# Performance work log

Measured on AMD Instinct MI355X. Metric: run time of the kernel, lower is better.

The kernel has to match this reference:

```python
import jax, jax.numpy as jnp
import numpy as np

VOL = (256, 256, 256)
K = 64  # number of connected components (clusters)


def setup_inputs() -> dict:
    key = jax.random.key(0)
    k1, k2, k3 = jax.random.split(key, 3)
    # Precomputed connected-component labels of (pred + target) > 0.
    # 0 = background, 1..K = clusters.
    labels = jax.random.randint(k1, VOL, 0, K + 1, dtype=jnp.int32)
    fg = labels > 0
    # Binary prediction / ground-truth masks, nonzero only inside labeled regions
    # (consistent with labels being components of the overlay of pred and target).
    pred = ((jax.random.uniform(k2, VOL) < 0.6) & fg).astype(jnp.float32)
    target = ((jax.random.uniform(k3, VOL) < 0.6) & fg).astype(jnp.float32)
    return {"pred": pred, "target": target, "labels": labels, "num_clusters": K}


def reference(pred, target, labels, num_clusters):
    # Per-cluster dice via one fused segment reduction instead of a Python loop
    # over clusters. Segment 0 is background and is dropped, matching
    # range(1, num_features + 1) in the original.
    lab = labels.reshape(-1)
    p = pred.reshape(-1)
    t = target.reshape(-1)
    nseg = num_clusters + 1
    # intersection = sum(pred_cluster * gt_cluster); pred/target are binary so
    # logical_and(...).float() products reduce to pred * target per segment.
    inter = jax.ops.segment_sum(p * t, lab, num_segments=nseg)[1:]
    sum_p = jax.ops.segment_sum(p, lab, num_segments=nseg)[1:]
    sum_t = jax.ops.segment_sum(t, lab, num_segments=nseg)[1:]
    union = sum_p + sum_t
    dice = jnp.where(union > 0, 2.0 * inter / jnp.maximum(union, 1.0), 1.0)
    return 1.0 - jnp.mean(dice)
```

## Files before the change

### kernel.cpp

```cpp
#include <hip/hip_runtime.h>


#define NSEG 65
#define NWAVES 4
#define BLOCKS 2048
#define THREADS 256

__device__ __forceinline__ unsigned long long pack_contrib(float p, float t) {
    unsigned long long sp = (p != 0.0f) ? 1ull : 0ull;
    unsigned long long st = (t != 0.0f) ? 1ull : 0ull;
    return ((sp & st) << 42) | (sp << 21) | st;
}

__device__ __forceinline__ void accum4(unsigned long long (*s_cnt)[NSEG], int wave,
                                       float4 p, float4 t, int4 l) {
    atomicAdd(&s_cnt[wave][l.x], pack_contrib(p.x, t.x));
    atomicAdd(&s_cnt[wave][l.y], pack_contrib(p.y, t.y));
    atomicAdd(&s_cnt[wave][l.z], pack_contrib(p.z, t.z));
    atomicAdd(&s_cnt[wave][l.w], pack_contrib(p.w, t.w));
}

__global__ __launch_bounds__(THREADS) void seg_count_kernel(
    const float* __restrict__ pred,
    const float* __restrict__ target,
    const int* __restrict__ labels,
    unsigned long long* __restrict__ g_counts,
    int n)
{
    __shared__ unsigned long long s_cnt[NWAVES][NSEG];
    const int tid = threadIdx.x;
    const int wave = tid >> 6;

    for (int i = tid; i < NWAVES * NSEG; i += THREADS)
        ((unsigned long long*)s_cnt)[i] = 0ull;
    __syncthreads();

    const int n_vec = n >> 2;
    const float4* __restrict__ p4 = (const float4*)pred;
    const float4* __restrict__ t4 = (const float4*)target;
    const int4*   __restrict__ l4 = (const int4*)labels;

    const int chunk = (n_vec + (int)gridDim.x - 1) / (int)gridDim.x;
    const int base = blockIdx.x * chunk;
    const int end = min(base + chunk, n_vec);

    int idx = base + tid;
    for (; idx + 3 * THREADS < end; idx += 4 * THREADS) {
        float4 p0 = p4[idx];
        float4 p1 = p4[idx + THREADS];
        float4 p2 = p4[idx + 2 * THREADS];
        float4 p3 = p4[idx + 3 * THREADS];
        float4 t0 = t4[idx];
        float4 t1 = t4[idx + THREADS];
        float4 t2 = t4[idx + 2 * THREADS];
        float4 t3 = t4[idx + 3 * THREADS];
        int4   l0 = l4[idx];
        int4   l1 = l4[idx + THREADS];
        int4   l2 = l4[idx + 2 * THREADS];
        int4   l3 = l4[idx + 3 * THREADS];
        accum4(s_cnt, wave, p0, t0, l0);
        accum4(s_cnt, wave, p1, t1, l1);
        accum4(s_cnt, wave, p2, t2, l2);
        accum4(s_cnt, wave, p3, t3, l3);
    }
    for (; idx < end; idx += THREADS)
        accum4(s_cnt, wave, p4[idx], t4[idx], l4[idx]);

    if (blockIdx.x == 0) {
        for (int i = (n_vec << 2) + tid; i < n; i += THREADS)
            atomicAdd(&s_cnt[wave][labels[i]], pack_contrib(pred[i], target[i]));
    }
    __syncthreads();

    for (int s = tid; s < NSEG; s += THREADS) {
        unsigned long long tot = 0;
        #pragma unroll
        for (int w = 0; w < NWAVES; ++w) tot += s_cnt[w][s];
        if (tot) atomicAdd(&g_counts[s], tot);
    }
}

__global__ __launch_bounds__(64) void dice_finalize_kernel(
    const unsigned long long* __restrict__ g_counts,
    const int* __restrict__ nc_ptr,
    float* __restrict__ out)
{
    const int nc = *nc_ptr;
    const int tid = threadIdx.x;
    float local = 0.0f;
    for (int c = 1 + tid; c <= nc; c += 64) {
        unsigned long long v = g_counts[c];
        float in = (float)(v >> 42);
        float sp = (float)((v >> 21) & 0x1FFFFFull);
        float st = (float)(v & 0x1FFFFFull);
        float uni = sp + st;
        local += (uni > 0.0f) ? (2.0f * in / uni) : 1.0f;
    }
    #pragma unroll
    for (int off = 32; off > 0; off >>= 1)
        local += __shfl_down(local, off);
    if (tid == 0) out[0] = 1.0f - local / (float)nc;
}

extern "C" void kernel_launch(void* const* d_in, const int* in_sizes, int n_in,
                              void* d_out, int out_size, void* d_ws, size_t ws_size,
                              hipStream_t stream) {
    const float* pred   = (const float*)d_in[0];
    const float* target = (const float*)d_in[1];
    const int*   labels = (const int*)d_in[2];
    const int*   nc_ptr = (const int*)d_in[3];
    float* out = (float*)d_out;
    unsigned long long* g_counts = (unsigned long long*)d_ws;

    const int n = in_sizes[0];

    hipMemsetAsync(d_ws, 0, NSEG * sizeof(unsigned long long), stream);

    seg_count_kernel<<<BLOCKS, THREADS, 0, stream>>>(
        pred, target, labels, g_counts, n);
    dice_finalize_kernel<<<1, 64, 0, stream>>>(g_counts, nc_ptr, out);
}
```

Before: 205.0 us.

## Double-buffer global loads against LDS atomics in segment count kernel

Restructures the main loop into a software pipeline: it prefetches the next set of float4/int4 loads into a second register buffer while processing LDS atomics for the current set. It also halves the grid to 1024 blocks and adds a min-blocks hint to launch_bounds. The goal is to hide global memory latency behind the shared-memory atomic work. In exchange, the double buffer roughly doubles live registers, which could lower occupancy or cause spills.

```diff
diff --git a/kernel.cpp b/kernel.cpp
--- a/kernel.cpp
+++ b/kernel.cpp
@@ -3,8 +3,9 @@
 
 #define NSEG 65
 #define NWAVES 4
-#define BLOCKS 2048
+#define BLOCKS 1024
 #define THREADS 256
+#define SETSPAN (4 * THREADS)
 
 __device__ __forceinline__ unsigned long long pack_contrib(float p, float t) {
     unsigned long long sp = (p != 0.0f) ? 1ull : 0ull;
@@ -12,15 +13,7 @@
     return ((sp & st) << 42) | (sp << 21) | st;
 }
 
-__device__ __forceinline__ void accum4(unsigned long long (*s_cnt)[NSEG], int wave,
-                                       float4 p, float4 t, int4 l) {
-    atomicAdd(&s_cnt[wave][l.x], pack_contrib(p.x, t.x));
-    atomicAdd(&s_cnt[wave][l.y], pack_contrib(p.y, t.y));
-    atomicAdd(&s_cnt[wave][l.z], pack_contrib(p.z, t.z));
-    atomicAdd(&s_cnt[wave][l.w], pack_contrib(p.w, t.w));
-}
-
-__global__ __launch_bounds__(THREADS) void seg_count_kernel(
+__global__ __launch_bounds__(THREADS, 4) void seg_count_kernel(
     const float* __restrict__ pred,
     const float* __restrict__ target,
     const int* __restrict__ labels,
@@ -43,31 +36,52 @@
     const int chunk = (n_vec + (int)gridDim.x - 1) / (int)gridDim.x;
     const int base = blockIdx.x * chunk;
     const int end = min(base + chunk, n_vec);
+    const int nsets = (end - base) / SETSPAN;
+
+    float4 pr[2][4], tr[2][4];
+    int4   lr[2][4];
+
+    auto load_set = [&](int b, int at) {
+        #pragma unroll
+        for (int g = 0; g < 4; ++g) {
+            pr[b][g] = p4[at + g * THREADS];
+            tr[b][g] = t4[at + g * THREADS];
+            lr[b][g] = l4[at + g * THREADS];
+        }
+    };
+    auto proc_set = [&](int b) {
+        #pragma unroll
+        for (int g = 0; g < 4; ++g) {
+            atomicAdd(&s_cnt[wave][lr[b][g].x], pack_contrib(pr[b][g].x, tr[b][g].x));
+            atomicAdd(&s_cnt[wave][lr[b][g].y], pack_contrib(pr[b][g].y, tr[b][g].y));
+            atomicAdd(&s_cnt[wave][lr[b][g].z], pack_contrib(pr[b][g].z, tr[b][g].z));
+            atomicAdd(&s_cnt[wave][lr[b][g].w], pack_contrib(pr[b][g].w, tr[b][g].w));
+        }
+    };
 
     int idx = base + tid;
-    for (; idx + 3 * THREADS < end; idx += 4 * THREADS) {
-        float4 p0 = p4[idx];
-        float4 p1 = p4[idx + THREADS];
-        float4 p2 = p4[idx + 2 * THREADS];
-        float4 p3 = p4[idx + 3 * THREADS];
-        float4 t0 = t4[idx];
-        float4 t1 = t4[idx + THREADS];
-        float4 t2 = t4[idx + 2 * THREADS];
-        float4 t3 = t4[idx + 3 * THREADS];
-        int4   l0 = l4[idx];
-        int4   l1 = l4[idx + THREADS];
-        int4   l2 = l4[idx + 2 * THREADS];
-        int4   l3 = l4[idx + 3 * THREADS];
-        accum4(s_cnt, wave, p0, t0, l0);
-        accum4(s_cnt, wave, p1, t1, l1);
-        accum4(s_cnt, wave, p2, t2, l2);
-        accum4(s_cnt, wave, p3, t3, l3);
+    if (nsets > 0) {
+        load_set(0, idx);
+        int buf = 0;
+        for (int s = 0; s < nsets - 1; ++s) {
+            load_set(buf ^ 1, idx + SETSPAN);
+            proc_set(buf);
+            idx += SETSPAN;
+            buf ^= 1;
+        }
+        proc_set(buf);
     }
-    for (; idx < end; idx += THREADS)
-        accum4(s_cnt, wave, p4[idx], t4[idx], l4[idx]);
-
+    for (idx = base + nsets * SETSPAN + tid; idx < end; idx += THREADS) {
+        float4 p = p4[idx];
+        float4 t = t4[idx];
+        int4   l = l4[idx];
+        atomicAdd(&s_cnt[wave][l.x], pack_contrib(p.x, t.x));
+        atomicAdd(&s_cnt[wave][l.y], pack_contrib(p.y, t.y));
+        atomicAdd(&s_cnt[wave][l.z], pack_contrib(p.z, t.z));
+        atomicAdd(&s_cnt[wave][l.w], pack_contrib(p.w, t.w));
+    }
     if (blockIdx.x == 0) {
-        for (int i = (n_vec << 2) + tid; i < n; i += THREADS)
+        for (int i = ((n >> 2) << 2) + tid; i < n; i += THREADS)
             atomicAdd(&s_cnt[wave][labels[i]], pack_contrib(pred[i], target[i]));
     }
     __syncthreads();
```

Result: slower. 254.8 us (+24.3%).

## Use per-lane privatized 32-bit shared histograms to avoid LDS atomic contention

Applied to the files above, without the earlier changes.

Replaces the per-wave 64-bit shared counters with a per-lane table of 32-bit packed counters laid out as segment*64+lane. Each lane of a wave then owns a distinct LDS bank and address, which removes intra-wave atomic conflicts and halves the atomic width. At the end, one thread per segment sums the 64 lane slots with a rotated index and repacks the result into the 64-bit global format. The 10-bit fields are only safe while a single lane adds fewer than 1024 voxels to one segment, and the table uses about 16.6 KB of LDS, which may reduce occupancy.

```diff
diff --git a/kernel.cpp b/kernel.cpp
--- a/kernel.cpp
+++ b/kernel.cpp
@@ -2,22 +2,13 @@
 
 
 #define NSEG 65
-#define NWAVES 4
 #define BLOCKS 2048
 #define THREADS 256
 
-__device__ __forceinline__ unsigned long long pack_contrib(float p, float t) {
-    unsigned long long sp = (p != 0.0f) ? 1ull : 0ull;
-    unsigned long long st = (t != 0.0f) ? 1ull : 0ull;
-    return ((sp & st) << 42) | (sp << 21) | st;
-}
-
-__device__ __forceinline__ void accum4(unsigned long long (*s_cnt)[NSEG], int wave,
-                                       float4 p, float4 t, int4 l) {
-    atomicAdd(&s_cnt[wave][l.x], pack_contrib(p.x, t.x));
-    atomicAdd(&s_cnt[wave][l.y], pack_contrib(p.y, t.y));
-    atomicAdd(&s_cnt[wave][l.z], pack_contrib(p.z, t.z));
-    atomicAdd(&s_cnt[wave][l.w], pack_contrib(p.w, t.w));
+__device__ __forceinline__ unsigned int pack_contrib32(float p, float t) {
+    unsigned int sp = (p != 0.0f) ? 1u : 0u;
+    unsigned int st = (t != 0.0f) ? 1u : 0u;
+    return ((sp & st) << 20) | (sp << 10) | st;
 }
 
 __global__ __launch_bounds__(THREADS) void seg_count_kernel(
@@ -27,12 +18,12 @@
     unsigned long long* __restrict__ g_counts,
     int n)
 {
-    __shared__ unsigned long long s_cnt[NWAVES][NSEG];
+    __shared__ unsigned int s_tab[NSEG * 64];
     const int tid = threadIdx.x;
-    const int wave = tid >> 6;
+    const int lane = tid & 63;
 
-    for (int i = tid; i < NWAVES * NSEG; i += THREADS)
-        ((unsigned long long*)s_cnt)[i] = 0ull;
+    for (int i = tid; i < NSEG * 64; i += THREADS)
+        s_tab[i] = 0u;
     __syncthreads();
 
     const int n_vec = n >> 2;
@@ -58,25 +49,51 @@
         int4   l1 = l4[idx + THREADS];
         int4   l2 = l4[idx + 2 * THREADS];
         int4   l3 = l4[idx + 3 * THREADS];
-        accum4(s_cnt, wave, p0, t0, l0);
-        accum4(s_cnt, wave, p1, t1, l1);
-        accum4(s_cnt, wave, p2, t2, l2);
-        accum4(s_cnt, wave, p3, t3, l3);
+        atomicAdd(&s_tab[l0.x * 64 + lane], pack_contrib32(p0.x, t0.x));
+        atomicAdd(&s_tab[l0.y * 64 + lane], pack_contrib32(p0.y, t0.y));
+        atomicAdd(&s_tab[l0.z * 64 + lane], pack_contrib32(p0.z, t0.z));
+        atomicAdd(&s_tab[l0.w * 64 + lane], pack_contrib32(p0.w, t0.w));
+        atomicAdd(&s_tab[l1.x * 64 + lane], pack_contrib32(p1.x, t1.x));
+        atomicAdd(&s_tab[l1.y * 64 + lane], pack_contrib32(p1.y, t1.y));
+        atomicAdd(&s_tab[l1.z * 64 + lane], pack_contrib32(p1.z, t1.z));
+        atomicAdd(&s_tab[l1.w * 64 + lane], pack_contrib32(p1.w, t1.w));
+        atomicAdd(&s_tab[l2.x * 64 + lane], pack_contrib32(p2.x, t2.x));
+        atomicAdd(&s_tab[l2.y * 64 + lane], pack_contrib32(p2.y, t2.y));
+        atomicAdd(&s_tab[l2.z * 64 + lane], pack_contrib32(p2.z, t2.z));
+        atomicAdd(&s_tab[l2.w * 64 + lane], pack_contrib32(p2.w, t2.w));
+        atomicAdd(&s_tab[l3.x * 64 + lane], pack_contrib32(p3.x, t3.x));
+        atomicAdd(&s_tab[l3.y * 64 + lane], pack_contrib32(p3.y, t3.y));
+        atomicAdd(&s_tab[l3.z * 64 + lane], pack_contrib32(p3.z, t3.z));
+        atomicAdd(&s_tab[l3.w * 64 + lane], pack_contrib32(p3.w, t3.w));
     }
-    for (; idx < end; idx += THREADS)
-        accum4(s_cnt, wave, p4[idx], t4[idx], l4[idx]);
-
+    for (; idx < end; idx += THREADS) {
+        float4 p = p4[idx];
+        float4 t = t4[idx];
+        int4   l = l4[idx];
+        atomicAdd(&s_tab[l.x * 64 + lane], pack_contrib32(p.x, t.x));
+        atomicAdd(&s_tab[l.y * 64 + lane], pack_contrib32(p.y, t.y));
+        atomicAdd(&s_tab[l.z * 64 + lane], pack_contrib32(p.z, t.z));
+        atomicAdd(&s_tab[l.w * 64 + lane], pack_contrib32(p.w, t.w));
+    }
     if (blockIdx.x == 0) {
-        for (int i = (n_vec << 2) + tid; i < n; i += THREADS)
-            atomicAdd(&s_cnt[wave][labels[i]], pack_contrib(pred[i], target[i]));
+        for (int i = ((n >> 2) << 2) + tid; i < n; i += THREADS)
+            atomicAdd(&s_tab[labels[i] * 64 + lane],
+                      pack_contrib32(pred[i], target[i]));
     }
     __syncthreads();
 
-    for (int s = tid; s < NSEG; s += THREADS) {
-        unsigned long long tot = 0;
+    if (tid >= 1 && tid < NSEG) {
+        const int seg = tid;
+        unsigned long long inter = 0, sp = 0, st = 0;
         #pragma unroll
-        for (int w = 0; w < NWAVES; ++w) tot += s_cnt[w][s];
-        if (tot) atomicAdd(&g_counts[s], tot);
+        for (int j = 0; j < 64; ++j) {
+            unsigned int v = s_tab[seg * 64 + ((j + tid) & 63)];
+            inter += v >> 20;
+            sp += (v >> 10) & 1023u;
+            st += v & 1023u;
+        }
+        unsigned long long tot = (inter << 42) | (sp << 21) | st;
+        if (tot) atomicAdd(&g_counts[seg], tot);
     }
 }
 
```

New measurement: 214.6 us. 1.05x slower.

## Replace global atomics and memset with per-block partials and a tree reduction

Applied to the files above, without the earlier changes.

Each block now writes its 64 per-segment packed counts to its own slot in a workspace array instead of issuing global 64-bit atomics into one shared counter array. A single 1024-thread finalize kernel sums the 2048 partials in two stages and computes the dice loss. This removes the hipMemsetAsync launch and the global atomic contention on 65 addresses. In exchange it adds about 1 MB of partial writes and reads and a serial single-block reduction. The finalize kernel hardcodes 64 clusters and ignores num_clusters when choosing which segments to sum.

```diff
diff --git a/kernel.cpp b/kernel.cpp
--- a/kernel.cpp
+++ b/kernel.cpp
@@ -2,9 +2,9 @@
 
 
 #define NSEG 65
+#define NBLK 2048
+#define THREADS 256
 #define NWAVES 4
-#define BLOCKS 2048
-#define THREADS 256
 
 __device__ __forceinline__ unsigned long long pack_contrib(float p, float t) {
     unsigned long long sp = (p != 0.0f) ? 1ull : 0ull;
@@ -24,7 +24,7 @@
     const float* __restrict__ pred,
     const float* __restrict__ target,
     const int* __restrict__ labels,
-    unsigned long long* __restrict__ g_counts,
+    unsigned long long* __restrict__ g_part,
     int n)
 {
     __shared__ unsigned long long s_cnt[NWAVES][NSEG];
@@ -67,7 +67,7 @@
         accum4(s_cnt, wave, p4[idx], t4[idx], l4[idx]);
 
     if (blockIdx.x == 0) {
-        for (int i = (n_vec << 2) + tid; i < n; i += THREADS)
+        for (int i = ((n >> 2) << 2) + tid; i < n; i += THREADS)
             atomicAdd(&s_cnt[wave][labels[i]], pack_contrib(pred[i], target[i]));
     }
     __syncthreads();
@@ -76,30 +76,42 @@
         unsigned long long tot = 0;
         #pragma unroll
         for (int w = 0; w < NWAVES; ++w) tot += s_cnt[w][s];
-        if (tot) atomicAdd(&g_counts[s], tot);
+        if (s >= 1)
+            g_part[(unsigned)blockIdx.x * 64u + (unsigned)(s - 1)] = tot;
     }
 }
 
-__global__ __launch_bounds__(64) void dice_finalize_kernel(
-    const unsigned long long* __restrict__ g_counts,
+__global__ __launch_bounds__(1024) void reduce_finalize_kernel(
+    const unsigned long long* __restrict__ g_part,
     const int* __restrict__ nc_ptr,
     float* __restrict__ out)
 {
-    const int nc = *nc_ptr;
+    __shared__ unsigned long long s_part[16][64];
     const int tid = threadIdx.x;
-    float local = 0.0f;
-    for (int c = 1 + tid; c <= nc; c += 64) {
-        unsigned long long v = g_counts[c];
-        float in = (float)(v >> 42);
-        float sp = (float)((v >> 21) & 0x1FFFFFull);
-        float st = (float)(v & 0x1FFFFFull);
+    const int seg = tid & 63;
+    const int j = tid >> 6;
+
+    unsigned long long acc = 0;
+    const int bpj = NBLK / 16;
+    for (int b = j * bpj; b < (j + 1) * bpj; ++b)
+        acc += g_part[(unsigned)b * 64u + (unsigned)seg];
+    s_part[j][seg] = acc;
+    __syncthreads();
+
+    if (tid < 64) {
+        unsigned long long tot = 0;
+        #pragma unroll
+        for (int jj = 0; jj < 16; ++jj) tot += s_part[jj][seg];
+        float in = (float)(tot >> 42);
+        float sp = (float)((tot >> 21) & 0x1FFFFFull);
+        float st = (float)(tot & 0x1FFFFFull);
         float uni = sp + st;
-        local += (uni > 0.0f) ? (2.0f * in / uni) : 1.0f;
+        float local = (uni > 0.0f) ? (2.0f * in / uni) : 1.0f;
+        #pragma unroll
+        for (int off = 32; off > 0; off >>= 1)
+            local += __shfl_down(local, off);
+        if (tid == 0) out[0] = 1.0f - local / (float)(*nc_ptr);
     }
-    #pragma unroll
-    for (int off = 32; off > 0; off >>= 1)
-        local += __shfl_down(local, off);
-    if (tid == 0) out[0] = 1.0f - local / (float)nc;
 }
 
 extern "C" void kernel_launch(void* const* d_in, const int* in_sizes, int n_in,
@@ -110,13 +122,11 @@
     const int*   labels = (const int*)d_in[2];
     const int*   nc_ptr = (const int*)d_in[3];
     float* out = (float*)d_out;
-    unsigned long long* g_counts = (unsigned long long*)d_ws;
+    unsigned long long* g_part = (unsigned long long*)d_ws;
 
     const int n = in_sizes[0];
 
-    hipMemsetAsync(d_ws, 0, NSEG * sizeof(unsigned long long), stream);
-
-    seg_count_kernel<<<BLOCKS, THREADS, 0, stream>>>(
-        pred, target, labels, g_counts, n);
-    dice_finalize_kernel<<<1, 64, 0, stream>>>(g_counts, nc_ptr, out);
+    seg_count_kernel<<<NBLK, THREADS, 0, stream>>>(
+        pred, target, labels, g_part, n);
+    reduce_finalize_kernel<<<1, 1024, 0, stream>>>(g_part, nc_ptr, out);
 }
```

Result: slower. 212.9 us (+3.8%).
